# Kernel optimization log

Hardware: AMD Instinct MI355X
Metric: run time of the kernel (lower is better)

Reference implementation:

```python
import jax, jax.numpy as jnp
import numpy as np

B, CIN, COUT, H, W, K = 8, 128, 128, 32, 32, 3
FULL = K * K  # 9 kernel taps
EPS = 1e-7


def inv3(b):
    # batched closed-form 3x3 inverse via adjugate, matching torch inverse3 (det + eps)
    b00, b01, b02 = b[:, 0, 0], b[:, 0, 1], b[:, 0, 2]
    b10, b11, b12 = b[:, 1, 0], b[:, 1, 1], b[:, 1, 2]
    b20, b21, b22 = b[:, 2, 0], b[:, 2, 1], b[:, 2, 2]
    det = (b00 * (b11 * b22 - b12 * b21)
           - b01 * (b10 * b22 - b12 * b20)
           + b02 * (b10 * b21 - b11 * b20)) + EPS
    c = jnp.stack([
        b11 * b22 - b12 * b21, b02 * b21 - b01 * b22, b01 * b12 - b02 * b11,
        b12 * b20 - b10 * b22, b00 * b22 - b02 * b20, b02 * b10 - b00 * b12,
        b10 * b21 - b11 * b20, b01 * b20 - b00 * b21, b00 * b11 - b01 * b10,
    ], axis=-1)  # (N, 9)
    return (c / det[:, None]).reshape(-1, 3, 3)


def cayley_kernels(kernel):
    # kernel: (16,) params -> per-tap 3x3 Cayley matrices G (9,3,3)
    # torch loop: num = i except i==8 -> kern//2 = 1; i==4 -> identity; a = b = kernel[2*num], c = kernel[2*num+1]
    nums = jnp.array([0, 1, 2, 3, 0, 5, 6, 7, 1])
    a = kernel[2 * nums]
    c = kernel[2 * nums + 1]
    o = jnp.ones_like(a)
    # first[i] = [[1,-a,-a],[a,1,-c],[a,c,1]]
    F = jnp.stack([o, -a, -a, a, o, -c, a, c, o], axis=-1).reshape(FULL, 3, 3)
    eye = jnp.eye(3, dtype=kernel.dtype)
    F = F.at[4].set(eye)
    S = 2.0 * eye - F  # second = sign-flipped off-diagonals; S[4] = eye
    return jnp.matmul(inv3(F), S)  # (9,3,3)


def setup_inputs() -> dict:
    key = jax.random.key(0)
    k1, k2 = jax.random.split(key)
    x = jax.random.normal(k1, (B, CIN, H, W, 3, 3), dtype=jnp.float32)
    g = jax.random.uniform(k2, ((FULL - 1) * 2 + CIN * COUT,), dtype=jnp.float32) - 0.5
    return {"x": x, "g": g}


def reference(x, g):
    kernel = g[:(FULL - 1) * 2]
    G = cayley_kernels(kernel)  # (9,3,3), tap t = kh*3 + kw
    # y[b,c,h,w,t,i,j] = (G_t @ X @ G_t^T)[i,j]
    y = jnp.einsum('tip,bchwpq,tjq->bcthwij', G, x, G)
    Ho, Wo = H + K - 1, W + K - 1
    # fold: matrix-element index (mi,mj) acts as the 3x3 spatial offset (layout aliasing in torch code);
    # kernel tap t stays a channel sub-index -> folded[b,c,t, h+mi, w+mj] += y[b,c,t,h,w,mi,mj]
    folded = jnp.zeros((B, CIN, FULL, Ho, Wo), dtype=y.dtype)
    for mi in range(3):
        for mj in range(3):
            folded = folded.at[:, :, :, mi:mi + H, mj:mj + W].add(y[..., mi, mj])
    # channel mixing with squared (nonneg) weights
    c_mat = (g[(FULL - 1) * 2:] ** 2).reshape(CIN, COUT)
    mixed = jnp.einsum('bcthw,co->bothw', folded, c_mat)  # (B,COUT,9,Ho,Wo)
    out = jnp.transpose(mixed, (0, 1, 3, 4, 2)).reshape(B, COUT, Ho, Wo, 3, 3)
    result = 0.5 * (out + jnp.swapaxes(out, -1, -2))
    return result
```

## Files before the change

kernel.cpp:

```cpp
#include <hip/hip_runtime.h>

#define NB    8
#define CIN   128
#define COUT  128
#define HH    32
#define WW    32
#define HO    34
#define WO    34
#define SSP   (HO*WO)
#define SPAD  1160
#define UU    6
#define NS    (SPAD*UU)
#define NT    48
#define EPSC  1e-7f

typedef __attribute__((ext_vector_type(8))) short bf16x8;
typedef __attribute__((ext_vector_type(4))) float f32x4;

__device__ __forceinline__ ushort f2b(float f) {
  uint u = __float_as_uint(f);
  uint r = (u + 0x7fffu + ((u >> 16) & 1u)) >> 16;
  return (ushort)r;
}

__global__ void prep_kernel(const float* __restrict__ g,
                            float* __restrict__ M,
                            ushort* __restrict__ wT) {
  if (blockIdx.x == 0) {
    __shared__ float Gs[81];
    int t = threadIdx.x;
    if (t < 9) {
      const int nums[9] = {0,1,2,3,0,5,6,7,1};
      float a = g[2*nums[t]];
      float c = g[2*nums[t]+1];
      float F[9], S2[9];
      if (t == 4) {
        F[0]=1;F[1]=0;F[2]=0;F[3]=0;F[4]=1;F[5]=0;F[6]=0;F[7]=0;F[8]=1;
        S2[0]=1;S2[1]=0;S2[2]=0;S2[3]=0;S2[4]=1;S2[5]=0;S2[6]=0;S2[7]=0;S2[8]=1;
      } else {
        F[0]=1.f; F[1]=-a;  F[2]=-a;
        F[3]=a;   F[4]=1.f; F[5]=-c;
        F[6]=a;   F[7]=c;   F[8]=1.f;
        S2[0]=1.f;  S2[1]=a;   S2[2]=a;
        S2[3]=-a;   S2[4]=1.f; S2[5]=c;
        S2[6]=-a;   S2[7]=-c;  S2[8]=1.f;
      }
      float det = F[0]*(F[4]*F[8]-F[5]*F[7]) - F[1]*(F[3]*F[8]-F[5]*F[6])
                + F[2]*(F[3]*F[7]-F[4]*F[6]) + EPSC;
      float inv[9];
      inv[0] = (F[4]*F[8]-F[5]*F[7]);
      inv[1] = (F[2]*F[7]-F[1]*F[8]);
      inv[2] = (F[1]*F[5]-F[2]*F[4]);
      inv[3] = (F[5]*F[6]-F[3]*F[8]);
      inv[4] = (F[0]*F[8]-F[2]*F[6]);
      inv[5] = (F[2]*F[3]-F[0]*F[5]);
      inv[6] = (F[3]*F[7]-F[4]*F[6]);
      inv[7] = (F[1]*F[6]-F[0]*F[7]);
      inv[8] = (F[0]*F[4]-F[1]*F[3]);
      float rd = 1.0f/det;
      #pragma unroll
      for (int i = 0; i < 9; ++i) inv[i] *= rd;
      #pragma unroll
      for (int i = 0; i < 3; ++i)
        #pragma unroll
        for (int j = 0; j < 3; ++j)
          Gs[t*9+i*3+j] = inv[i*3+0]*S2[0*3+j] + inv[i*3+1]*S2[1*3+j] + inv[i*3+2]*S2[2*3+j];
    }
    __syncthreads();
    if (t < 6) {
      const int T1[6] = {0,1,2,4,5,8};
      const int T2[6] = {0,3,6,4,7,8};
      int t1 = T1[t], t2 = T2[t];
      for (int co = 0; co < 9; ++co) {
        int i = co/3, j = co%3;
        for (int k = 0; k < 9; ++k) {
          int p = k/3, q = k%3;
          M[t*81 + co*9 + k] =
            0.5f*(Gs[t1*9+i*3+p]*Gs[t1*9+j*3+q] + Gs[t2*9+i*3+p]*Gs[t2*9+j*3+q]);
        }
      }
    }
  } else {
    int idx = (int)(blockIdx.x-1)*256 + threadIdx.x;
    int o = idx >> 7, c = idx & 127;
    float w = g[16 + c*128 + o];
    wT[idx] = f2b(w*w);
  }
}

__global__ __launch_bounds__(256) void fold_kernel(const float* __restrict__ x,
                                                   const float* __restrict__ M,
                                                   ushort* __restrict__ folded) {
  __shared__ float Y[1024*9];
  int tid = threadIdx.x;
  const float* xb = x + (size_t)blockIdx.x * (HH*WW*9);

  float X[4][9];
  #pragma unroll
  for (int kk = 0; kk < 4; ++kk) {
    int loc = tid + kk*256;
    #pragma unroll
    for (int i = 0; i < 9; ++i) X[kk][i] = xb[loc*9 + i];
  }

  size_t ob = (size_t)blockIdx.x * NS;

  for (int u = 0; u < 6; ++u) {
    if (u) __syncthreads();
    const float* Mu = M + u*81;
    #pragma unroll
    for (int co = 0; co < 9; ++co) {
      float m[9];
      #pragma unroll
      for (int k = 0; k < 9; ++k) m[k] = Mu[co*9 + k];
      #pragma unroll
      for (int kk = 0; kk < 4; ++kk) {
        float y = m[0]*X[kk][0];
        #pragma unroll
        for (int k = 1; k < 9; ++k) y += m[k]*X[kk][k];
        Y[(tid + kk*256)*9 + co] = y;
      }
    }
    __syncthreads();

    #pragma unroll
    for (int r = 0; r < 5; ++r) {
      int idx = tid + r*256;
      if (idx < SSP) {
        uint ho = (uint)idx / 34u;
        uint wo = (uint)idx - 34u*ho;
        float acc = 0.f;
        #pragma unroll
        for (int i = 0; i < 3; ++i) {
          int hh = (int)ho - i;
          bool okh = (uint)hh < 32u;
          #pragma unroll
          for (int j = 0; j < 3; ++j) {
            int wwj = (int)wo - j;
            bool ok = okh && ((uint)wwj < 32u);
            int px = hh*32 + wwj;
            px = min(max(px, 0), 1023);
            float v = Y[px*9 + i*3 + j];
            acc += ok ? v : 0.f;
          }
        }
        folded[ob + (size_t)idx*6 + u] = f2b(acc);
      }
    }
  }
}

__global__ __launch_bounds__(192) void gemm_kernel(const ushort* __restrict__ wT,
                                                   const ushort* __restrict__ folded,
                                                   float* __restrict__ out) {
  __shared__ __align__(16) char smem[128*52*4];
  ushort* ldsB = (ushort*)smem;
  float*  ldsC = (float*)smem;

  int tid  = threadIdx.x;
  int b    = blockIdx.y;
  int tile = blockIdx.x;
  int n0   = tile * NT;

  #pragma unroll
  for (int p = 0; p < 4; ++p) {
    int chunk = tid + p*192;
    int c  = chunk / 6;
    int nc = (chunk - 6*c) * 8;
    const ushort* src = folded + ((size_t)(b*CIN + c)*NS + n0 + nc);
    uint4 v = *(const uint4*)src;
    ushort e[8];
    e[0]=(ushort)(v.x & 0xffffu); e[1]=(ushort)(v.x >> 16);
    e[2]=(ushort)(v.y & 0xffffu); e[3]=(ushort)(v.y >> 16);
    e[4]=(ushort)(v.z & 0xffffu); e[5]=(ushort)(v.z >> 16);
    e[6]=(ushort)(v.w & 0xffffu); e[7]=(ushort)(v.w >> 16);
    #pragma unroll
    for (int j = 0; j < 8; ++j) {
      int nl  = nc + j;
      int ksw = c ^ (((nl >> 3) & 7) << 4);
      ldsB[nl*136 + ksw] = e[j];
    }
  }
  __syncthreads();

  int wave = tid >> 6, lane = tid & 63;
  int l15 = lane & 15, lhi = lane >> 4;
  int nl = wave*16 + l15;
  int sw = ((nl >> 3) & 7) << 4;

  f32x4 acc[8];
  #pragma unroll
  for (int i = 0; i < 8; ++i) acc[i] = (f32x4){0.f,0.f,0.f,0.f};

  const ushort* wrow = wT + l15*128;
  #pragma unroll
  for (int k0 = 0; k0 < 128; k0 += 32) {
    int kk = k0 + lhi*8;
    bf16x8 bfrag = *(const bf16x8*)&ldsB[nl*136 + (kk ^ sw)];
    #pragma unroll
    for (int mf = 0; mf < 8; ++mf) {
      bf16x8 afrag = *(const bf16x8*)(wrow + mf*16*128 + kk);
      acc[mf] = __builtin_amdgcn_mfma_f32_16x16x32_bf16(afrag, bfrag, acc[mf], 0, 0, 0);
    }
  }

  __syncthreads();
  #pragma unroll
  for (int mf = 0; mf < 8; ++mf)
    #pragma unroll
    for (int r = 0; r < 4; ++r) {
      int o = mf*16 + lhi*4 + r;
      ldsC[o*52 + nl] = acc[mf][r];
    }
  __syncthreads();

  int s0 = tile * 8;
  const int umap[9] = {0,1,2,1,3,4,2,4,5};
  #pragma unroll
  for (int r = 0; r < 6; ++r) {
    int pair = tid + r*192;
    if (pair < 1024) {
      int o  = pair >> 3;
      int sl = pair & 7;
      int s  = s0 + sl;
      if (s < SSP) {
        float v[6];
        #pragma unroll
        for (int u = 0; u < 6; ++u) v[u] = ldsC[o*52 + sl*6 + u];
        size_t base = ((size_t)(b*COUT + o)*SSP + s)*9;
        #pragma unroll
        for (int t = 0; t < 9; ++t) out[base + t] = v[umap[t]];
      }
    }
  }
}

extern "C" void kernel_launch(void* const* d_in, const int* in_sizes, int n_in,
                              void* d_out, int out_size, void* d_ws, size_t ws_size,
                              hipStream_t stream) {
  const float* x = (const float*)d_in[0];
  const float* g = (const float*)d_in[1];
  float* out = (float*)d_out;

  float*  M      = (float*)d_ws;
  ushort* wT     = (ushort*)((char*)d_ws + 4096);
  ushort* folded = (ushort*)((char*)d_ws + 4096 + 32768);

  prep_kernel<<<65, 256, 0, stream>>>(g, M, wT);
  fold_kernel<<<NB*CIN, 256, 0, stream>>>(x, M, folded);
  gemm_kernel<<<dim3(NS/NT, NB), 192, 0, stream>>>(wT, folded, out);
}
```

Before: 138.1 us.

## Fuse tap transform into gather in fold kernel, store packed bf16 outputs

The fold kernel now stages raw x in shared memory and, for each output pixel and each of the 9 offsets, gathers the neighbouring input matrix and applies the per-tap transform on the fly. This replaces the six-pass compute-Y/sync/fold loop and its large Y buffer. The identity tap (u=3) becomes a plain element pick instead of a dot product. Outputs are written as packed pairs of bf16 in three 32-bit stores per pixel, and padded entries are zero-filled. In exchange it repeats the transform for each offset, adding arithmetic and register pressure (30 accumulators plus 45 coefficients).

```diff
diff --git a/kernel.cpp b/kernel.cpp
--- a/kernel.cpp
+++ b/kernel.cpp
@@ -91,61 +91,89 @@
 __global__ __launch_bounds__(256) void fold_kernel(const float* __restrict__ x,
                                                    const float* __restrict__ M,
                                                    ushort* __restrict__ folded) {
-  __shared__ float Y[1024*9];
+  __shared__ float4 XsA[1024];
+  __shared__ float4 XsB[1024];
+  __shared__ float  XsC[1024];
   int tid = threadIdx.x;
   const float* xb = x + (size_t)blockIdx.x * (HH*WW*9);
 
-  float X[4][9];
   #pragma unroll
   for (int kk = 0; kk < 4; ++kk) {
-    int loc = tid + kk*256;
-    #pragma unroll
-    for (int i = 0; i < 9; ++i) X[kk][i] = xb[loc*9 + i];
-  }
-
-  size_t ob = (size_t)blockIdx.x * NS;
-
-  for (int u = 0; u < 6; ++u) {
-    if (u) __syncthreads();
-    const float* Mu = M + u*81;
-    #pragma unroll
-    for (int co = 0; co < 9; ++co) {
-      float m[9];
-      #pragma unroll
-      for (int k = 0; k < 9; ++k) m[k] = Mu[co*9 + k];
-      #pragma unroll
-      for (int kk = 0; kk < 4; ++kk) {
-        float y = m[0]*X[kk][0];
-        #pragma unroll
-        for (int k = 1; k < 9; ++k) y += m[k]*X[kk][k];
-        Y[(tid + kk*256)*9 + co] = y;
-      }
-    }
-    __syncthreads();
-
-    #pragma unroll
-    for (int r = 0; r < 5; ++r) {
-      int idx = tid + r*256;
-      if (idx < SSP) {
-        uint ho = (uint)idx / 34u;
-        uint wo = (uint)idx - 34u*ho;
-        float acc = 0.f;
-        #pragma unroll
-        for (int i = 0; i < 3; ++i) {
-          int hh = (int)ho - i;
-          bool okh = (uint)hh < 32u;
+    int px = tid + kk*256;
+    const float* p = xb + px*9;
+    float v0=p[0],v1=p[1],v2=p[2],v3=p[3],v4=p[4],v5=p[5],v6=p[6],v7=p[7],v8=p[8];
+    XsA[px] = make_float4(v0,v1,v2,v3);
+    XsB[px] = make_float4(v4,v5,v6,v7);
+    XsC[px] = v8;
+  }
+  __syncthreads();
+
+  float acc[5][6];
+  #pragma unroll
+  for (int r = 0; r < 5; ++r)
+    #pragma unroll
+    for (int u = 0; u < 6; ++u) acc[r][u] = 0.f;
+
+  int hoA[5], woA[5];
+  #pragma unroll
+  for (int r = 0; r < 5; ++r) {
+    int idx = tid + r*256;
+    uint hh = (uint)idx / 34u;
+    hoA[r] = (int)hh;
+    woA[r] = idx - 34*(int)hh;
+  }
+
+  const int ulist[5] = {0,1,2,4,5};
+  #pragma unroll
+  for (int i = 0; i < 3; ++i) {
+    #pragma unroll
+    for (int j = 0; j < 3; ++j) {
+      float m[5][9];
+      #pragma unroll
+      for (int uu = 0; uu < 5; ++uu)
+        #pragma unroll
+        for (int k = 0; k < 9; ++k)
+          m[uu][k] = M[ulist[uu]*81 + (i*3+j)*9 + k];
+
+      #pragma unroll
+      for (int r = 0; r < 5; ++r) {
+        int idx = tid + r*256;
+        if (r < 4 || idx < SSP) {
+          int hh = hoA[r] - i;
+          int wj = woA[r] - j;
+          bool ok = ((uint)hh < 32u) && ((uint)wj < 32u);
+          int px = hh*32 + wj;
+          px = min(max(px, 0), 1023);
+          float4 a = XsA[px];
+          float4 b = XsB[px];
+          float  c = XsC[px];
+          float v[9] = {a.x,a.y,a.z,a.w,b.x,b.y,b.z,b.w,c};
           #pragma unroll
-          for (int j = 0; j < 3; ++j) {
-            int wwj = (int)wo - j;
-            bool ok = okh && ((uint)wwj < 32u);
-            int px = hh*32 + wwj;
-            px = min(max(px, 0), 1023);
-            float v = Y[px*9 + i*3 + j];
-            acc += ok ? v : 0.f;
+          for (int k = 0; k < 9; ++k) v[k] = ok ? v[k] : 0.f;
+          acc[r][3] += v[i*3+j];
+          #pragma unroll
+          for (int uu = 0; uu < 5; ++uu) {
+            float d = m[uu][0]*v[0];
+            #pragma unroll
+            for (int k = 1; k < 9; ++k) d = fmaf(m[uu][k], v[k], d);
+            acc[r][ulist[uu]] += d;
           }
         }
-        folded[ob + (size_t)idx*6 + u] = f2b(acc);
-      }
+      }
+    }
+  }
+
+  uint* outp = (uint*)folded + (size_t)blockIdx.x * (NS/2);
+  #pragma unroll
+  for (int r = 0; r < 5; ++r) {
+    int idx = tid + r*256;
+    if (idx < SPAD) {
+      uint p0 = (uint)f2b(acc[r][0]) | ((uint)f2b(acc[r][1]) << 16);
+      uint p1 = (uint)f2b(acc[r][2]) | ((uint)f2b(acc[r][3]) << 16);
+      uint p2 = (uint)f2b(acc[r][4]) | ((uint)f2b(acc[r][5]) << 16);
+      outp[idx*3+0] = p0;
+      outp[idx*3+1] = p1;
+      outp[idx*3+2] = p2;
     }
   }
 }
```

Result: slower. 159.9 us (+15.8%).
